# Kernel tuning notes

Hardware: AMD Instinct MI355X
Metric: run time of the kernel (lower is better)

Reference implementation:

```python
import jax, jax.numpy as jnp
import numpy as np
from jax import lax

FLAT = 2 * 2 * 16  # 64, conv output flattened channel-major like torch .view


def setup_inputs() -> dict:
    key = jax.random.key(0)
    ks = jax.random.split(key, 12)
    s = 0.1
    # board with values in {-1, 0, 1} so the legality mask is nontrivial
    x = jax.random.randint(ks[0], (1, 1, 3, 3), -1, 2).astype(jnp.float32)
    return {
        "x": x,
        "conv_w": jax.random.normal(ks[1], (16, 1, 2, 2), jnp.float32) * s,
        "fc_w": jax.random.normal(ks[2], (32, FLAT), jnp.float32) * s,
        "fc_b": jax.random.normal(ks[3], (32,), jnp.float32) * s,
        "a1_w": jax.random.normal(ks[4], (16, 32), jnp.float32) * s,
        "a1_b": jax.random.normal(ks[5], (16,), jnp.float32) * s,
        "a2_w": jax.random.normal(ks[6], (9, 16), jnp.float32) * s,
        "a2_b": jax.random.normal(ks[7], (9,), jnp.float32) * s,
        "v1_w": jax.random.normal(ks[8], (8, 32), jnp.float32) * s,
        "v1_b": jax.random.normal(ks[9], (8,), jnp.float32) * s,
        "v2_w": jax.random.normal(ks[10], (1, 8), jnp.float32) * s,
        "v2_b": jax.random.normal(ks[11], (1,), jnp.float32) * s,
    }


def reference(x, conv_w, fc_w, fc_b, a1_w, a1_b, a2_w, a2_b, v1_w, v1_b, v2_w, v2_b):
    # conv(1->16, k=2, stride=1, no bias) on [1,1,3,3] -> [1,16,2,2]
    y = lax.conv_general_dilated(
        x, conv_w, window_strides=(1, 1), padding="VALID",
        dimension_numbers=("NCHW", "OIHW", "NCHW"))
    y = jax.nn.relu(y).reshape(-1, FLAT)          # [1,64], channel-major flatten
    y = jax.nn.relu(y @ fc_w.T + fc_b)            # [1,32]

    a = jax.nn.relu(y @ a1_w.T + a1_b)            # [1,16]
    a = a @ a2_w.T + a2_b                         # [1,9] action logits

    # legality mask: cells not occupied (|x| != 1)
    avail = (jnp.abs(jnp.squeeze(x)) != 1).astype(jnp.float32).reshape(-1, 9)
    maxa = jnp.max(a)                             # global max (batch of 1)
    e = avail * jnp.exp(a - maxa)
    prob = e / jnp.sum(e)                         # masked softmax, [1,9]

    v = jax.nn.relu(y @ v1_w.T + v1_b)            # [1,8]
    value = jnp.tanh(v @ v2_w.T + v2_b)           # [1,1]
    return (prob.reshape(3, 3), value)
```

## Files before the change

kernel.cpp:

```cpp
#include <hip/hip_runtime.h>
#include <math.h>


__global__ __launch_bounds__(64) void policy3x3_kernel(
    const float* __restrict__ x,
    const float* __restrict__ conv_w,
    const float* __restrict__ fc_w,
    const float* __restrict__ fc_b,
    const float* __restrict__ a1_w,
    const float* __restrict__ a1_b,
    const float* __restrict__ a2_w,
    const float* __restrict__ a2_b,
    const float* __restrict__ v1_w,
    const float* __restrict__ v1_b,
    const float* __restrict__ v2_w,
    const float* __restrict__ v2_b,
    float* __restrict__ out)
{
    __shared__ float s_x[9];
    __shared__ float s_f[64];
    __shared__ float s_y[32];
    __shared__ float s_ah[16];
    __shared__ float s_vh[8];
    __shared__ float s_logit[9];

    const int t = threadIdx.x;

    if (t < 9) s_x[t] = x[t];
    __syncthreads();

    {
        const int oc  = t >> 2;
        const int pos = t & 3;
        const int oh  = pos >> 1;
        const int ow  = pos & 1;
        float acc = 0.f;
#pragma unroll
        for (int kh = 0; kh < 2; ++kh)
#pragma unroll
            for (int kw = 0; kw < 2; ++kw)
                acc += s_x[(oh + kh) * 3 + (ow + kw)] * conv_w[oc * 4 + kh * 2 + kw];
        s_f[t] = fmaxf(acc, 0.f);
    }
    __syncthreads();

    if (t < 32) {
        float acc = fc_b[t];
#pragma unroll
        for (int k = 0; k < 64; ++k)
            acc += s_f[k] * fc_w[t * 64 + k];
        s_y[t] = fmaxf(acc, 0.f);
    }
    __syncthreads();

    if (t < 16) {
        float acc = a1_b[t];
#pragma unroll
        for (int j = 0; j < 32; ++j)
            acc += s_y[j] * a1_w[t * 32 + j];
        s_ah[t] = fmaxf(acc, 0.f);
    } else if (t < 24) {
        const int i = t - 16;
        float acc = v1_b[i];
#pragma unroll
        for (int j = 0; j < 32; ++j)
            acc += s_y[j] * v1_w[i * 32 + j];
        s_vh[i] = fmaxf(acc, 0.f);
    }
    __syncthreads();

    if (t < 9) {
        float acc = a2_b[t];
#pragma unroll
        for (int i = 0; i < 16; ++i)
            acc += s_ah[i] * a2_w[t * 16 + i];
        s_logit[t] = acc;
    }
    __syncthreads();

    if (t == 0) {
        float maxa = s_logit[0];
#pragma unroll
        for (int c = 1; c < 9; ++c) maxa = fmaxf(maxa, s_logit[c]);
        float e[9];
        float sum = 0.f;
#pragma unroll
        for (int c = 0; c < 9; ++c) {
            const float avail = (fabsf(s_x[c]) != 1.0f) ? 1.0f : 0.0f;
            e[c] = avail * __expf(s_logit[c] - maxa);
            sum += e[c];
        }
        const float inv = 1.0f / sum;
#pragma unroll
        for (int c = 0; c < 9; ++c) out[c] = e[c] * inv;
    } else if (t == 1) {
        float acc = v2_b[0];
#pragma unroll
        for (int i = 0; i < 8; ++i)
            acc += s_vh[i] * v2_w[i];
        out[9] = tanhf(acc);
    }
}

extern "C" void kernel_launch(void* const* d_in, const int* in_sizes, int n_in,
                              void* d_out, int out_size, void* d_ws, size_t ws_size,
                              hipStream_t stream) {
    (void)in_sizes; (void)n_in; (void)d_ws; (void)ws_size; (void)out_size;
    const float* x      = (const float*)d_in[0];
    const float* conv_w = (const float*)d_in[1];
    const float* fc_w   = (const float*)d_in[2];
    const float* fc_b   = (const float*)d_in[3];
    const float* a1_w   = (const float*)d_in[4];
    const float* a1_b   = (const float*)d_in[5];
    const float* a2_w   = (const float*)d_in[6];
    const float* a2_b   = (const float*)d_in[7];
    const float* v1_w   = (const float*)d_in[8];
    const float* v1_b   = (const float*)d_in[9];
    const float* v2_w   = (const float*)d_in[10];
    const float* v2_b   = (const float*)d_in[11];
    float* out = (float*)d_out;

    hipLaunchKernelGGL(policy3x3_kernel, dim3(1), dim3(64), 0, stream,
                       x, conv_w, fc_w, fc_b, a1_w, a1_b, a2_w, a2_b,
                       v1_w, v1_b, v2_w, v2_b, out);
}
```

Baseline: 76.77 us.

## Prefetch all weights into registers upfront with float4 loads and split FC across wave

All layer weights are loaded with vectorized float4 reads into registers at kernel start, before the first barrier, so global-memory latency overlaps instead of being serialized per layer. The 64-wide FC dot product is split across both halves of the wavefront and combined with a shuffle. The value-head output is computed one stage earlier on a separate lane. Register pressure rises, and float4 loads assume the weight buffers are 16-byte aligned.

```diff
diff --git a/kernel.cpp b/kernel.cpp
--- a/kernel.cpp
+++ b/kernel.cpp
@@ -26,55 +26,99 @@
 
     const int t = threadIdx.x;
 
+    const float4 cw = ((const float4*)conv_w)[t >> 2];
+
+    const int r = t & 31;
+    const int h = t >> 5;
+    float4 fw[8];
+    {
+        const float4* p = (const float4*)fc_w + r * 16 + h * 8;
+#pragma unroll
+        for (int i = 0; i < 8; ++i) fw[i] = p[i];
+    }
+    const float fb = fc_b[r];
+
+    float4 hw[8];
+    float  hb = 0.f;
+    if (t < 16) {
+        const float4* p = (const float4*)a1_w + t * 8;
+#pragma unroll
+        for (int i = 0; i < 8; ++i) hw[i] = p[i];
+        hb = a1_b[t];
+    } else if (t < 24) {
+        const float4* p = (const float4*)v1_w + (t - 16) * 8;
+#pragma unroll
+        for (int i = 0; i < 8; ++i) hw[i] = p[i];
+        hb = v1_b[t - 16];
+    } else if (t < 33) {
+        const float4* p = (const float4*)a2_w + (t - 24) * 4;
+#pragma unroll
+        for (int i = 0; i < 4; ++i) hw[i] = p[i];
+        hb = a2_b[t - 24];
+    } else if (t == 34) {
+        hw[0] = ((const float4*)v2_w)[0];
+        hw[1] = ((const float4*)v2_w)[1];
+        hb = v2_b[0];
+    }
+
     if (t < 9) s_x[t] = x[t];
     __syncthreads();
 
     {
-        const int oc  = t >> 2;
         const int pos = t & 3;
         const int oh  = pos >> 1;
         const int ow  = pos & 1;
-        float acc = 0.f;
-#pragma unroll
-        for (int kh = 0; kh < 2; ++kh)
-#pragma unroll
-            for (int kw = 0; kw < 2; ++kw)
-                acc += s_x[(oh + kh) * 3 + (ow + kw)] * conv_w[oc * 4 + kh * 2 + kw];
-        s_f[t] = fmaxf(acc, 0.f);
+        float f = cw.x * s_x[oh * 3 + ow]
+                + cw.y * s_x[oh * 3 + ow + 1]
+                + cw.z * s_x[(oh + 1) * 3 + ow]
+                + cw.w * s_x[(oh + 1) * 3 + ow + 1];
+        s_f[t] = fmaxf(f, 0.f);
     }
     __syncthreads();
 
-    if (t < 32) {
-        float acc = fc_b[t];
+    {
+        float acc = 0.f;
+        const float* sf = s_f + h * 32;
 #pragma unroll
-        for (int k = 0; k < 64; ++k)
-            acc += s_f[k] * fc_w[t * 64 + k];
-        s_y[t] = fmaxf(acc, 0.f);
+        for (int i = 0; i < 8; ++i)
+            acc += fw[i].x * sf[i * 4 + 0] + fw[i].y * sf[i * 4 + 1]
+                 + fw[i].z * sf[i * 4 + 2] + fw[i].w * sf[i * 4 + 3];
+        acc += __shfl_xor(acc, 32);
+        s_y[r] = fmaxf(acc + fb, 0.f);
     }
     __syncthreads();
 
     if (t < 16) {
-        float acc = a1_b[t];
+        float a = hb;
 #pragma unroll
-        for (int j = 0; j < 32; ++j)
-            acc += s_y[j] * a1_w[t * 32 + j];
-        s_ah[t] = fmaxf(acc, 0.f);
+        for (int i = 0; i < 8; ++i)
+            a += hw[i].x * s_y[i * 4 + 0] + hw[i].y * s_y[i * 4 + 1]
+               + hw[i].z * s_y[i * 4 + 2] + hw[i].w * s_y[i * 4 + 3];
+        s_ah[t] = fmaxf(a, 0.f);
     } else if (t < 24) {
-        const int i = t - 16;
-        float acc = v1_b[i];
+        float a = hb;
 #pragma unroll
-        for (int j = 0; j < 32; ++j)
-            acc += s_y[j] * v1_w[i * 32 + j];
-        s_vh[i] = fmaxf(acc, 0.f);
+        for (int i = 0; i < 8; ++i)
+            a += hw[i].x * s_y[i * 4 + 0] + hw[i].y * s_y[i * 4 + 1]
+               + hw[i].z * s_y[i * 4 + 2] + hw[i].w * s_y[i * 4 + 3];
+        s_vh[t - 16] = fmaxf(a, 0.f);
     }
     __syncthreads();
 
-    if (t < 9) {
-        float acc = a2_b[t];
+    if (t >= 24 && t < 33) {
+        float a = hb;
 #pragma unroll
-        for (int i = 0; i < 16; ++i)
-            acc += s_ah[i] * a2_w[t * 16 + i];
-        s_logit[t] = acc;
+        for (int i = 0; i < 4; ++i)
+            a += hw[i].x * s_ah[i * 4 + 0] + hw[i].y * s_ah[i * 4 + 1]
+               + hw[i].z * s_ah[i * 4 + 2] + hw[i].w * s_ah[i * 4 + 3];
+        s_logit[t - 24] = a;
+    } else if (t == 34) {
+        float a = hb;
+        a += hw[0].x * s_vh[0] + hw[0].y * s_vh[1]
+           + hw[0].z * s_vh[2] + hw[0].w * s_vh[3];
+        a += hw[1].x * s_vh[4] + hw[1].y * s_vh[5]
+           + hw[1].z * s_vh[6] + hw[1].w * s_vh[7];
+        out[9] = tanhf(a);
     }
     __syncthreads();
 
@@ -93,12 +137,6 @@
         const float inv = 1.0f / sum;
 #pragma unroll
         for (int c = 0; c < 9; ++c) out[c] = e[c] * inv;
-    } else if (t == 1) {
-        float acc = v2_b[0];
-#pragma unroll
-        for (int i = 0; i < 8; ++i)
-            acc += s_vh[i] * v2_w[i];
-        out[9] = tanhf(acc);
     }
 }
 
```

Measured after the change: 77.22 us. About the same (+0.6%).
